# Kernel optimization log

Hardware: AMD Instinct MI355X
Metric: run time of the kernel (lower is better)

The kernel has to match this reference:

```python
import jax, jax.numpy as jnp
import numpy as np

INPUT_DIM = 1024
ATTN_DIM = 512
N1 = 4096
N2 = 4096


def setup_inputs() -> dict:
    key = jax.random.key(0)
    ks = jax.random.split(key, 10)
    s_in = 1.0 / np.sqrt(INPUT_DIM)   # torch Linear default init scale
    s_at = 1.0 / np.sqrt(ATTN_DIM)
    return {
        "input1": jax.random.normal(ks[0], (N1, INPUT_DIM), jnp.float32),
        "input2": jax.random.normal(ks[1], (N2, INPUT_DIM), jnp.float32),
        "Wq": jax.random.uniform(ks[2], (INPUT_DIM, ATTN_DIM), jnp.float32, -s_in, s_in),
        "bq": jax.random.uniform(ks[3], (ATTN_DIM,), jnp.float32, -s_in, s_in),
        "Wk": jax.random.uniform(ks[4], (INPUT_DIM, ATTN_DIM), jnp.float32, -s_in, s_in),
        "bk": jax.random.uniform(ks[5], (ATTN_DIM,), jnp.float32, -s_in, s_in),
        "Wv": jax.random.uniform(ks[6], (INPUT_DIM, ATTN_DIM), jnp.float32, -s_in, s_in),
        "bv": jax.random.uniform(ks[7], (ATTN_DIM,), jnp.float32, -s_in, s_in),
        "Wo": jax.random.uniform(ks[8], (ATTN_DIM, INPUT_DIM), jnp.float32, -s_at, s_at),
        "bo": jax.random.uniform(ks[9], (INPUT_DIM,), jnp.float32, -s_at, s_at),
    }


def reference(input1, input2, Wq, bq, Wk, bk, Wv, bv, Wo, bo):
    # shared projections for both inputs
    q1 = input1 @ Wq + bq            # [N1, A]
    q2 = input2 @ Wq + bq            # [N2, A]
    k1 = input1 @ Wk + bk
    k2 = input2 @ Wk + bk
    v1 = input1 @ Wv + bv
    v2 = input2 @ Wv + bv
    # cross attention 1: input1 queries attend to input2 keys/values
    attn1 = jax.nn.softmax(q1 @ k2.T, axis=-1)   # [N1, N2]
    attn2 = jax.nn.softmax(q2 @ k1.T, axis=-1)   # [N2, N1]
    out1 = (attn1 @ v2) @ Wo + bo                # [N1, input_dim]
    out2 = (attn2 @ v1) @ Wo + bo                # [N2, input_dim]
    return (out1, out2)
```

## Files before the change

### kernel.cpp

```cpp
#include <hip/hip_runtime.h>

typedef __bf16 bf16;
typedef _Float16 f16;
typedef __bf16 bf16x8 __attribute__((ext_vector_type(8)));
typedef _Float16 f16x8 __attribute__((ext_vector_type(8)));
typedef _Float16 f16x4 __attribute__((ext_vector_type(4)));
typedef float f32x4 __attribute__((ext_vector_type(4)));

#define NROWS 4096
#define DIN 1024
#define DA 512
#define NCHUNK 64

template <typename T> struct V8;
template <> struct V8<f16> { using type = f16x8; };
template <> struct V8<bf16> { using type = bf16x8; };

__device__ __forceinline__ f32x4 mfma16(f16x8 a, f16x8 b, f32x4 c) {
  return __builtin_amdgcn_mfma_f32_16x16x32_f16(a, b, c, 0, 0, 0);
}
__device__ __forceinline__ f32x4 mfma16(bf16x8 a, bf16x8 b, f32x4 c) {
  return __builtin_amdgcn_mfma_f32_16x16x32_bf16(a, b, c, 0, 0, 0);
}

__device__ __forceinline__ void gload_lds16(const void* g, void* l) {
  __builtin_amdgcn_global_load_lds((const __attribute__((address_space(1))) void*)g,
                                   (__attribute__((address_space(3))) void*)l, 16, 0, 0);
}

template <int N> __device__ __forceinline__ void vmcnt_wait() {
  if constexpr (N == 0) asm volatile("s_waitcnt vmcnt(0)" ::: "memory");
  else if constexpr (N == 1) asm volatile("s_waitcnt vmcnt(1)" ::: "memory");
  else if constexpr (N == 2) asm volatile("s_waitcnt vmcnt(2)" ::: "memory");
  else if constexpr (N == 3) asm volatile("s_waitcnt vmcnt(3)" ::: "memory");
  else if constexpr (N == 4) asm volatile("s_waitcnt vmcnt(4)" ::: "memory");
  else if constexpr (N == 5) asm volatile("s_waitcnt vmcnt(5)" ::: "memory");
  else if constexpr (N == 6) asm volatile("s_waitcnt vmcnt(6)" ::: "memory");
  else if constexpr (N == 8) asm volatile("s_waitcnt vmcnt(8)" ::: "memory");
  else static_assert(N == 0, "unsupported vmcnt");
}


__global__ void cast_kernel(const float* __restrict__ s1, const float* __restrict__ s2,
                            f16* __restrict__ d1, f16* __restrict__ d2, int n) {
  const float* s = blockIdx.z ? s2 : s1;
  f16* d = blockIdx.z ? d2 : d1;
  int i = (blockIdx.x * blockDim.x + threadIdx.x) * 4;
  if (i < n) {
    float4 v = *(const float4*)(s + i);
    f16x4 o;
    o[0] = (f16)v.x; o[1] = (f16)v.y; o[2] = (f16)v.z; o[3] = (f16)v.w;
    *(f16x4*)(d + i) = o;
  }
}

__global__ void transpose_f32(const float* __restrict__ w0, const float* __restrict__ w1,
                              const float* __restrict__ w2, f16* __restrict__ dst,
                              size_t dstride, int rows, int cols) {
  const float* s = blockIdx.z == 0 ? w0 : (blockIdx.z == 1 ? w1 : w2);
  f16* d = dst + (size_t)blockIdx.z * dstride;
  __shared__ float tile[32][33];
  int bc = blockIdx.x * 32, br = blockIdx.y * 32;
  int tx = threadIdx.x, ty = threadIdx.y;
  for (int i = ty; i < 32; i += 8)
    tile[i][tx] = s[(size_t)(br + i) * cols + bc + tx];
  __syncthreads();
  for (int i = ty; i < 32; i += 8)
    d[(size_t)(bc + i) * rows + br + tx] = (f16)tile[tx][i];
}

__global__ void transpose_b16(const bf16* __restrict__ src, size_t sstride,
                              bf16* __restrict__ dst, size_t dstride, int rows, int cols) {
  const bf16* s = src + (size_t)blockIdx.z * sstride;
  bf16* d = dst + (size_t)blockIdx.z * dstride;
  __shared__ float tile[32][33];
  int bc = blockIdx.x * 32, br = blockIdx.y * 32;
  int tx = threadIdx.x, ty = threadIdx.y;
  for (int i = ty; i < 32; i += 8)
    tile[i][tx] = (float)s[(size_t)(br + i) * cols + bc + tx];
  __syncthreads();
  for (int i = ty; i < 32; i += 8)
    d[(size_t)(bc + i) * rows + br + tx] = (bf16)tile[tx][i];
}

__global__ void rowsum_reduce(const float* __restrict__ prsP, float* __restrict__ prsT) {
  int i = blockIdx.x * 256 + threadIdx.x;
  int z = i >> 12, row = i & 4095;
  const float* p = prsP + (size_t)z * NCHUNK * NROWS + row;
  float s = 0.f;
#pragma unroll
  for (int j = 0; j < NCHUNK; ++j) s += p[(size_t)j * NROWS];
  prsT[i] = s;
}

__global__ void merge_kernel(const float* __restrict__ pO, const float* __restrict__ prsT,
                             f16* __restrict__ mid) {
  const size_t QS = (size_t)NROWS * DA;
  size_t e = ((size_t)blockIdx.x * blockDim.x + threadIdx.x) * 4;
  int z = (int)(e / QS);
  size_t rem = e - (size_t)z * QS;
  int row = (int)(rem / DA);
  float4 a = *(const float4*)(pO + (size_t)z * QS + rem);
  float4 b = *(const float4*)(pO + (size_t)(2 + z) * QS + rem);
  float inv = 1.0f / prsT[z * NROWS + row];
  f16x4 o;
  o[0] = (f16)((a.x + b.x) * inv);
  o[1] = (f16)((a.y + b.y) * inv);
  o[2] = (f16)((a.z + b.z) * inv);
  o[3] = (f16)((a.w + b.w) * inv);
  *(f16x4*)(mid + (size_t)z * QS + rem) = o;
}


template <typename TIN>
struct G8Args {
  const TIN* A[6];
  const TIN* B[6];
  const float* bias[6];
  void* C[6];
  float* rsO[6];
  int k0[6];
  int storebf[6];
  int lda, ldb, ldc;
};

template <typename TIN, int EPI, int BN, int NT, int BK = 64, int MINW = 1, int PH = 4>
__global__ __launch_bounds__(512, MINW) void g8(G8Args<TIN> args) {
  using vec8 = typename V8<TIN>::type;
  constexpr int NFR = BN / 64;
  constexpr int FPP = 8 / PH;
  constexpr int KK = BK / 32;
  constexpr int RB = BK * 2;
  constexpr int CPR = RB / 16;
  constexpr int SWM = CPR - 1;
  constexpr int SFT = (CPR == 4) ? 1 : 0;
  constexpr int ABUF = 256 * RB;
  constexpr int BBUF = BN * RB;
  constexpr int BUFSZ = ABUF + BBUF;
  constexpr int IPU = ABUF / 2 / 8192;
  __shared__ __align__(16) char smem[2 * BUFSZ];

  static_assert(PH == 4 || PH == 2, "PH in {2,4}");

  const int z = blockIdx.z;
  const TIN* __restrict__ A = args.A[z];
  const TIN* __restrict__ B = args.B[z];
  const int lda = args.lda, ldb = args.ldb;
  const int k0 = args.k0[z];

  int blkM, blkN;
  {
    const int gx = gridDim.x;
    const int nwg = gx * gridDim.y;
    const int lin = blockIdx.y * gx + blockIdx.x;
    const int q = nwg >> 3;
    const int nl = (lin & 7) * q + (lin >> 3);
    blkN = nl % gx;
    blkM = nl / gx;
  }

  const int tid = threadIdx.x;
  const int w = tid >> 6, lane = tid & 63;
  const int wm = w & 1, wn = w >> 1;
  const int lr = lane & 15, lh = lane >> 4;

  const TIN* Abase = A + (size_t)blkM * 256 * lda;
  const TIN* Bbase = B + (size_t)blkN * BN * ldb;

  f32x4 acc[8][NFR] = {};
  vec8 af[FPP][KK], bfr[NFR][KK];

#define SWZ(r_) (((r_) >> SFT) & SWM)
#define STAGE_A(buf, hf, kt)                                                    \
  {                                                                             \
    char* dst_ = smem + (buf)*BUFSZ + (hf)*(ABUF / 2);                          \
    const TIN* src_ = Abase + (size_t)((hf)*128) * lda + (kt);                  \
    _Pragma("unroll")                                                           \
    for (int i_ = 0; i_ < IPU; ++i_) {                                          \
      int c_ = i_ * 512 + tid;                                                  \
      int r_ = c_ / CPR, q_ = c_ % CPR;                                         \
      gload_lds16(src_ + (size_t)r_ * lda + ((q_ ^ SWZ(r_)) << 3),              \
                  dst_ + c_ * 16);                                              \
    }                                                                           \
  }
#define STAGE_B(buf, hf, kt)                                                    \
  {                                                                             \
    char* dst_ = smem + (buf)*BUFSZ + ABUF + (hf)*(ABUF / 2);                   \
    const TIN* src_ = Bbase + (size_t)((hf)*128) * ldb + (kt);                  \
    _Pragma("unroll")                                                           \
    for (int i_ = 0; i_ < IPU; ++i_) {                                          \
      int c_ = i_ * 512 + tid;                                                  \
      int r_ = c_ / CPR, q_ = c_ % CPR;                                         \
      gload_lds16(src_ + (size_t)r_ * ldb + ((q_ ^ SWZ(r_)) << 3),              \
                  dst_ + c_ * 16);                                              \
    }                                                                           \
  }
#define LDA_PHASE(buf, p)                                                       \
  {                                                                             \
    char* Ab_ = smem + (buf)*BUFSZ;                                             \
    _Pragma("unroll")                                                           \
    for (int fi_ = 0; fi_ < FPP; ++fi_) {                                       \
      int row_ = (((p)*FPP + fi_) * 2 + wm) * 16 + lr;                          \
      _Pragma("unroll")                                                         \
      for (int kk_ = 0; kk_ < KK; ++kk_) {                                      \
        int cc_ = (kk_ * 4 + lh) ^ SWZ(row_);                                   \
        af[fi_][kk_] = *(const vec8*)(Ab_ + row_ * RB + cc_ * 16);              \
      }                                                                         \
    }                                                                           \
  }
#define LDB_ALL(buf)                                                            \
  {                                                                             \
    char* Bb_ = smem + (buf)*BUFSZ + ABUF;                                      \
    _Pragma("unroll")                                                           \
    for (int n_ = 0; n_ < NFR; ++n_) {                                          \
      int row_ = wn * (BN / 4) + n_ * 16 + lr;                                  \
      _Pragma("unroll")                                                         \
      for (int kk_ = 0; kk_ < KK; ++kk_) {                                      \
        int cc_ = (kk_ * 4 + lh) ^ SWZ(row_);                                   \
        bfr[n_][kk_] = *(const vec8*)(Bb_ + row_ * RB + cc_ * 16);              \
      }                                                                         \
    }                                                                           \
  }
#define MFMA_PHASE(p)                                                           \
  {                                                                             \
    _Pragma("unroll")                                                           \
    for (int fi_ = 0; fi_ < FPP; ++fi_) {                                       \
      _Pragma("unroll")                                                         \
      for (int n_ = 0; n_ < NFR; ++n_) {                                        \
        _Pragma("unroll")                                                       \
        for (int kk_ = 0; kk_ < KK; ++kk_)                                      \
          acc[(p)*FPP + fi_][n_] = mfma16(af[fi_][kk_], bfr[n_][kk_],           \
                                          acc[(p)*FPP + fi_][n_]);              \
      }                                                                         \
    }                                                                           \
  }
#define BAR() __builtin_amdgcn_s_barrier()
#define LGK0()                                          \
  asm volatile("s_waitcnt lgkmcnt(0)" ::: "memory");    \
  __builtin_amdgcn_sched_barrier(0)

  if constexpr (NFR == 4) {
    STAGE_B(0, 0, k0); STAGE_B(0, 1, k0); STAGE_A(0, 0, k0); STAGE_A(0, 1, k0);
  } else {
    STAGE_B(0, 0, k0); STAGE_A(0, 0, k0); STAGE_A(0, 1, k0);
  }
  vmcnt_wait<IPU>();
  BAR();

  for (int t = 0; t < NT; ++t) {
    const int cur = t & 1, nxt = cur ^ 1;
    const int ktn = k0 + (t + 1) * BK;
    const bool st = (t < NT - 1);
    if constexpr (PH == 4) {
      if (st) { STAGE_B(nxt, 0, ktn); }
      LDB_ALL(cur);
      LDA_PHASE(cur, 0);
      BAR(); LGK0();
      __builtin_amdgcn_s_setprio(1); MFMA_PHASE(0); __builtin_amdgcn_s_setprio(0);
      BAR();
      if (st) { STAGE_B(nxt, 1, ktn); }
      LDA_PHASE(cur, 1);
      BAR(); LGK0();
      __builtin_amdgcn_s_setprio(1); MFMA_PHASE(1); __builtin_amdgcn_s_setprio(0);
      if (st) { vmcnt_wait<2 * IPU>(); }
      else    { vmcnt_wait<0>(); }
      BAR();
      if (st) { STAGE_A(nxt, 0, ktn); }
      LDA_PHASE(cur, 2);
      BAR(); LGK0();
      __builtin_amdgcn_s_setprio(1); MFMA_PHASE(2); __builtin_amdgcn_s_setprio(0);
      BAR();
      if (st) { STAGE_A(nxt, 1, ktn); }
      LDA_PHASE(cur, 3);
      BAR(); LGK0();
      __builtin_amdgcn_s_setprio(1); MFMA_PHASE(3); __builtin_amdgcn_s_setprio(0);
      if (st) { vmcnt_wait<IPU>(); }
      BAR();
    } else {
      if (st) {
        STAGE_B(nxt, 0, ktn);
        if constexpr (NFR == 4) { STAGE_B(nxt, 1, ktn); }
        STAGE_A(nxt, 0, ktn);
      }
      LDB_ALL(cur);
      LDA_PHASE(cur, 0);
      BAR(); LGK0();
      __builtin_amdgcn_s_setprio(1); MFMA_PHASE(0); __builtin_amdgcn_s_setprio(0);
      if (st) { vmcnt_wait<(NFR == 4 ? 3 : 2) * IPU>(); }
      else    { vmcnt_wait<0>(); }
      BAR();
      if (st) { STAGE_A(nxt, 1, ktn); }
      LDA_PHASE(cur, 1);
      BAR(); LGK0();
      __builtin_amdgcn_s_setprio(1); MFMA_PHASE(1); __builtin_amdgcn_s_setprio(0);
      if (st) { vmcnt_wait<IPU>(); }
      BAR();
    }
  }

  const int row0 = blkM * 256;
  const int col0 = blkN * BN + wn * (BN / 4);
  const int ldc = args.ldc;
  if constexpr (EPI == 1) {
#pragma unroll
    for (int a = 0; a < 8; ++a) {
      float rsv[4] = {0.f, 0.f, 0.f, 0.f};
#pragma unroll
      for (int n = 0; n < NFR; ++n) {
#pragma unroll
        for (int rr = 0; rr < 4; ++rr) {
          int row = row0 + (a * 2 + wm) * 16 + lh * 4 + rr;
          int col = col0 + n * 16 + lr;
          float e = __expf(acc[a][n][rr]);
          ((bf16*)args.C[z])[(size_t)row * ldc + col] = (bf16)e;
          rsv[rr] += e;
        }
      }
#pragma unroll
      for (int rr = 0; rr < 4; ++rr) {
        float s = rsv[rr];
        s += __shfl_xor(s, 1);
        s += __shfl_xor(s, 2);
        s += __shfl_xor(s, 4);
        s += __shfl_xor(s, 8);
        if (lr == 0) {
          int row = row0 + (a * 2 + wm) * 16 + lh * 4 + rr;
          args.rsO[z][((size_t)blkN * 4 + wn) * NROWS + row] = s;
        }
      }
    }
  } else {
#pragma unroll
    for (int a = 0; a < 8; ++a) {
#pragma unroll
      for (int n = 0; n < NFR; ++n) {
#pragma unroll
        for (int rr = 0; rr < 4; ++rr) {
          int row = row0 + (a * 2 + wm) * 16 + lh * 4 + rr;
          int col = col0 + n * 16 + lr;
          float v = acc[a][n][rr];
          if constexpr (EPI == 0) {
            float b = v + args.bias[z][col];
            if (args.storebf[z])
              ((bf16*)args.C[z])[(size_t)row * ldc + col] = (bf16)b;
            else
              ((f16*)args.C[z])[(size_t)row * ldc + col] = (f16)b;
          } else if constexpr (EPI == 2) {
            ((float*)args.C[z])[(size_t)row * ldc + col] = v;
          } else {
            ((float*)args.C[z])[(size_t)row * ldc + col] = v + args.bias[z][col];
          }
        }
      }
    }
  }
#undef SWZ
#undef STAGE_A
#undef STAGE_B
#undef LDA_PHASE
#undef LDB_ALL
#undef MFMA_PHASE
#undef BAR
#undef LGK0
}


extern "C" void kernel_launch(void* const* d_in, const int* in_sizes, int n_in,
                              void* d_out, int out_size, void* d_ws, size_t ws_size,
                              hipStream_t stream) {
  const float* in1 = (const float*)d_in[0];
  const float* in2 = (const float*)d_in[1];
  const float* Wq = (const float*)d_in[2];
  const float* bq = (const float*)d_in[3];
  const float* Wk = (const float*)d_in[4];
  const float* bk = (const float*)d_in[5];
  const float* Wv = (const float*)d_in[6];
  const float* bv = (const float*)d_in[7];
  const float* Wo = (const float*)d_in[8];
  const float* bo = (const float*)d_in[9];
  float* out = (float*)d_out;

  const size_t IN_E = (size_t)NROWS * DIN;
  const size_t WT_E = (size_t)DA * DIN;
  const size_t QS = (size_t)NROWS * DA;
  const size_t PS = (size_t)NROWS * NROWS;

  f16* qk = (f16*)d_ws;
  f16* in_hf = qk + 4 * QS;
  bf16* vv = (bf16*)(in_hf + 2 * IN_E);
  f16* wt = (f16*)(vv + 2 * QS);
  f16* woT = wt + 3 * WT_E;
  bf16* vt = (bf16*)(woT + WT_E);
  bf16* P = vt + 2 * QS;
  f16* mid = (f16*)(P + 2 * PS);
  float* pO = (float*)d_ws;
  float* prsP = (float*)vv;
  float* prsT = prsP + 2 * (size_t)NCHUNK * NROWS;

  cast_kernel<<<dim3((unsigned)(IN_E / 1024), 1, 2), dim3(256), 0, stream>>>(
      in1, in2, in_hf, in_hf + IN_E, (int)IN_E);

  transpose_f32<<<dim3(DA / 32, DIN / 32, 3), dim3(32, 8), 0, stream>>>(
      Wq, Wk, Wv, wt, WT_E, DIN, DA);
  transpose_f32<<<dim3(DIN / 32, DA / 32, 1), dim3(32, 8), 0, stream>>>(
      Wo, Wo, Wo, woT, 0, DA, DIN);

  {
    G8Args<f16> a{};
    const float* bs[3] = {bq, bk, bv};
    for (int zi = 0; zi < 6; ++zi) {
      int which = (zi < 4) ? (zi & 1) : 2;
      int src = (zi < 4) ? (zi >> 1) : (zi - 4);
      a.A[zi] = in_hf + (size_t)src * IN_E;
      a.B[zi] = wt + (size_t)which * WT_E;
      a.bias[zi] = bs[which];
      a.C[zi] = (zi < 4) ? (void*)(qk + (size_t)zi * QS) : (void*)(vv + (size_t)(zi - 4) * QS);
      a.storebf[zi] = (zi >= 4);
      a.k0[zi] = 0;
    }
    a.lda = DIN; a.ldb = DIN; a.ldc = DA;
    g8<f16, 0, 256, 16, 64, 1, 2><<<dim3(2, 16, 6), dim3(512), 0, stream>>>(a);
  }

  transpose_b16<<<dim3(DA / 32, NROWS / 32, 2), dim3(32, 8), 0, stream>>>(
      vv, QS, vt, QS, NROWS, DA);

  {
    G8Args<f16> a{};
    a.A[0] = qk + 0 * QS; a.B[0] = qk + 3 * QS; a.C[0] = P;
    a.A[1] = qk + 2 * QS; a.B[1] = qk + 1 * QS; a.C[1] = P + PS;
    a.rsO[0] = prsP;
    a.rsO[1] = prsP + (size_t)NCHUNK * NROWS;
    a.k0[0] = a.k0[1] = 0;
    a.lda = DA; a.ldb = DA; a.ldc = NROWS;
    g8<f16, 1, 256, 8, 64, 1, 2><<<dim3(16, 16, 2), dim3(512), 0, stream>>>(a);
  }

  rowsum_reduce<<<dim3(32), dim3(256), 0, stream>>>(prsP, prsT);

  {
    G8Args<bf16> a{};
    for (int i = 0; i < 4; ++i) {
      int pair = i & 1, s = i >> 1;
      a.A[i] = P + (size_t)pair * PS;
      a.B[i] = vt + (size_t)(pair ^ 1) * QS;
      a.C[i] = pO + (size_t)i * QS;
      a.k0[i] = s * 2048;
      a.storebf[i] = 0;
    }
    a.lda = NROWS; a.ldb = NROWS; a.ldc = DA;
    g8<bf16, 2, 128, 32, 64, 1, 2><<<dim3(4, 16, 4), dim3(512), 0, stream>>>(a);
  }

  merge_kernel<<<dim3((unsigned)(2 * QS / 1024)), dim3(256), 0, stream>>>(pO, prsT, mid);

  {
    G8Args<f16> a{};
    a.A[0] = mid;      a.C[0] = out;
    a.A[1] = mid + QS; a.C[1] = out + (size_t)NROWS * DIN;
    a.B[0] = a.B[1] = woT;
    a.bias[0] = a.bias[1] = bo;
    a.k0[0] = a.k0[1] = 0;
    a.lda = DA; a.ldb = DA; a.ldc = DIN;
    g8<f16, 3, 128, 8, 64, 1, 2><<<dim3(8, 16, 2), dim3(512), 0, stream>>>(a);
  }
}
```

Before: 203.7 us.

## Add dedicated QK^T exp kernel with 256x128 tiles and two blocks per CU

Replaces the generic g8 launch for the QK^T + exp + partial rowsum stage with a specialized kernel using 256x128 tiles, 48KB LDS, launch bounds allowing two blocks per CU, and a swizzled block order for L2 reuse. The column tile halves, so the number of partial rowsum chunks doubles (NCHUNK 64->128). The goal is more resident waves to hide latency and better scheduling of the exp-heavy epilogue. The cost is more blocks, reloading A tiles for every column block, and a larger rowsum reduction.

Result: slower. 233.0 us (+14.4%).

```diff
diff --git a/kernel.cpp b/kernel.cpp
--- a/kernel.cpp
+++ b/kernel.cpp
@@ -10,7 +10,7 @@
 #define NROWS 4096
 #define DIN 1024
 #define DA 512
-#define NCHUNK 64
+#define NCHUNK 128
 
 template <typename T> struct V8;
 template <> struct V8<f16> { using type = f16x8; };
@@ -109,6 +109,159 @@
   o[2] = (f16)((a.z + b.z) * inv);
   o[3] = (f16)((a.w + b.w) * inv);
   *(f16x4*)(mid + (size_t)z * QS + rem) = o;
+}
+
+
+__global__ __launch_bounds__(512, 2) void qk2(
+    const f16* __restrict__ q1, const f16* __restrict__ k2,
+    const f16* __restrict__ q2, const f16* __restrict__ k1,
+    bf16* __restrict__ Pout, float* __restrict__ prsP) {
+  __shared__ __align__(16) char smem[49152];
+  const int z = blockIdx.z;
+  const f16* __restrict__ A = z ? q2 : q1;
+  const f16* __restrict__ B = z ? k1 : k2;
+  bf16* __restrict__ C = Pout + (size_t)z * ((size_t)NROWS * NROWS);
+  float* __restrict__ rsO = prsP + (size_t)z * NCHUNK * NROWS;
+
+  int blkM, blkN;
+  {
+    const int lin = blockIdx.y * 32 + blockIdx.x;
+    const int nl = (lin & 7) * 64 + (lin >> 3);
+    blkN = nl & 31;
+    blkM = nl >> 5;
+  }
+
+  const int tid = threadIdx.x;
+  const int w = tid >> 6, lane = tid & 63;
+  const int wm = w & 1, wn = w >> 1;
+  const int lr = lane & 15, lh = lane >> 4;
+
+  const f16* Abase = A + (size_t)blkM * 256 * DA;
+  const f16* Bbase = B + (size_t)blkN * 128 * DA;
+
+  char* const bA0 = smem;
+  char* const bA1 = smem + 16384;
+  char* const bB = smem + 32768;
+
+  f32x4 acc[8][2] = {};
+  f16x8 af[4][2], bfr[2][2];
+
+#define STAGEU(dst_, src_)                                                      \
+  {                                                                             \
+    _Pragma("unroll")                                                           \
+    for (int i_ = 0; i_ < 2; ++i_) {                                            \
+      int c_ = i_ * 512 + tid;                                                  \
+      int r_ = c_ >> 3, q_ = c_ & 7;                                            \
+      gload_lds16((src_) + (size_t)r_ * DA + ((q_ ^ (r_ & 7)) << 3),            \
+                  (dst_) + c_ * 16);                                            \
+    }                                                                           \
+  }
+#define LDA_P(p)                                                                \
+  {                                                                             \
+    char* Ab_ = (p) ? bA1 : bA0;                                                \
+    _Pragma("unroll")                                                           \
+    for (int fi_ = 0; fi_ < 4; ++fi_) {                                         \
+      int grow_ = (((p)*4 + fi_) * 2 + wm) * 16 + lr;                           \
+      int row_ = grow_ & 127;                                                   \
+      _Pragma("unroll")                                                         \
+      for (int kk_ = 0; kk_ < 2; ++kk_) {                                       \
+        int cc_ = (kk_ * 4 + lh) ^ (row_ & 7);                                  \
+        af[fi_][kk_] = *(const f16x8*)(Ab_ + row_ * 128 + cc_ * 16);            \
+      }                                                                         \
+    }                                                                           \
+  }
+#define LDB_ALL()                                                               \
+  {                                                                             \
+    _Pragma("unroll")                                                           \
+    for (int n_ = 0; n_ < 2; ++n_) {                                            \
+      int row_ = wn * 32 + n_ * 16 + lr;                                        \
+      _Pragma("unroll")                                                         \
+      for (int kk_ = 0; kk_ < 2; ++kk_) {                                       \
+        int cc_ = (kk_ * 4 + lh) ^ (row_ & 7);                                  \
+        bfr[n_][kk_] = *(const f16x8*)(bB + row_ * 128 + cc_ * 16);             \
+      }                                                                         \
+    }                                                                           \
+  }
+#define MFMA_P(p)                                                               \
+  {                                                                             \
+    _Pragma("unroll")                                                           \
+    for (int fi_ = 0; fi_ < 4; ++fi_) {                                         \
+      _Pragma("unroll")                                                         \
+      for (int n_ = 0; n_ < 2; ++n_) {                                          \
+        _Pragma("unroll")                                                       \
+        for (int kk_ = 0; kk_ < 2; ++kk_)                                       \
+          acc[(p)*4 + fi_][n_] = mfma16(af[fi_][kk_], bfr[n_][kk_],             \
+                                        acc[(p)*4 + fi_][n_]);                  \
+      }                                                                         \
+    }                                                                           \
+  }
+#define BAR() __builtin_amdgcn_s_barrier()
+#define LGK0()                                          \
+  asm volatile("s_waitcnt lgkmcnt(0)" ::: "memory");    \
+  __builtin_amdgcn_sched_barrier(0)
+
+  STAGEU(bB, Bbase);
+  STAGEU(bA0, Abase);
+
+  for (int t = 0; t < 8; ++t) {
+    const int kt = t * 64;
+    const bool st = (t < 7);
+    STAGEU(bA1, Abase + (size_t)128 * DA + kt);
+    vmcnt_wait<2>();
+    BAR();
+    LDB_ALL();
+    LDA_P(0);
+    LGK0();
+    __builtin_amdgcn_s_setprio(1); MFMA_P(0); __builtin_amdgcn_s_setprio(0);
+    BAR();
+    if (st) {
+      STAGEU(bB, Bbase + kt + 64);
+      STAGEU(bA0, Abase + kt + 64);
+    }
+    if (st) { vmcnt_wait<4>(); }
+    else    { vmcnt_wait<0>(); }
+    BAR();
+    LDA_P(1);
+    LGK0();
+    __builtin_amdgcn_s_setprio(1); MFMA_P(1); __builtin_amdgcn_s_setprio(0);
+    BAR();
+  }
+
+  const int row0 = blkM * 256;
+  const int col0 = blkN * 128 + wn * 32;
+#pragma unroll
+  for (int a = 0; a < 8; ++a) {
+    float rsv[4] = {0.f, 0.f, 0.f, 0.f};
+#pragma unroll
+    for (int n = 0; n < 2; ++n) {
+#pragma unroll
+      for (int rr = 0; rr < 4; ++rr) {
+        int row = row0 + (a * 2 + wm) * 16 + lh * 4 + rr;
+        int col = col0 + n * 16 + lr;
+        float e = __expf(acc[a][n][rr]);
+        C[(size_t)row * NROWS + col] = (bf16)e;
+        rsv[rr] += e;
+      }
+    }
+#pragma unroll
+    for (int rr = 0; rr < 4; ++rr) {
+      float s = rsv[rr];
+      s += __shfl_xor(s, 1);
+      s += __shfl_xor(s, 2);
+      s += __shfl_xor(s, 4);
+      s += __shfl_xor(s, 8);
+      if (lr == 0) {
+        int row = row0 + (a * 2 + wm) * 16 + lh * 4 + rr;
+        rsO[((size_t)blkN * 4 + wn) * NROWS + row] = s;
+      }
+    }
+  }
+#undef STAGEU
+#undef LDA_P
+#undef LDB_ALL
+#undef MFMA_P
+#undef BAR
+#undef LGK0
 }
 
 
@@ -301,55 +454,25 @@
   const int row0 = blkM * 256;
   const int col0 = blkN * BN + wn * (BN / 4);
   const int ldc = args.ldc;
-  if constexpr (EPI == 1) {
-#pragma unroll
-    for (int a = 0; a < 8; ++a) {
-      float rsv[4] = {0.f, 0.f, 0.f, 0.f};
-#pragma unroll
-      for (int n = 0; n < NFR; ++n) {
-#pragma unroll
-        for (int rr = 0; rr < 4; ++rr) {
-          int row = row0 + (a * 2 + wm) * 16 + lh * 4 + rr;
-          int col = col0 + n * 16 + lr;
-          float e = __expf(acc[a][n][rr]);
-          ((bf16*)args.C[z])[(size_t)row * ldc + col] = (bf16)e;
-          rsv[rr] += e;
-        }
-      }
+#pragma unroll
+  for (int a = 0; a < 8; ++a) {
+#pragma unroll
+    for (int n = 0; n < NFR; ++n) {
 #pragma unroll
       for (int rr = 0; rr < 4; ++rr) {
-        float s = rsv[rr];
-        s += __shfl_xor(s, 1);
-        s += __shfl_xor(s, 2);
-        s += __shfl_xor(s, 4);
-        s += __shfl_xor(s, 8);
-        if (lr == 0) {
-          int row = row0 + (a * 2 + wm) * 16 + lh * 4 + rr;
-          args.rsO[z][((size_t)blkN * 4 + wn) * NROWS + row] = s;
-        }
-      }
-    }
-  } else {
-#pragma unroll
-    for (int a = 0; a < 8; ++a) {
-#pragma unroll
-      for (int n = 0; n < NFR; ++n) {
-#pragma unroll
-        for (int rr = 0; rr < 4; ++rr) {
-          int row = row0 + (a * 2 + wm) * 16 + lh * 4 + rr;
-          int col = col0 + n * 16 + lr;
-          float v = acc[a][n][rr];
-          if constexpr (EPI == 0) {
-            float b = v + args.bias[z][col];
-            if (args.storebf[z])
-              ((bf16*)args.C[z])[(size_t)row * ldc + col] = (bf16)b;
-            else
-              ((f16*)args.C[z])[(size_t)row * ldc + col] = (f16)b;
-          } else if constexpr (EPI == 2) {
-            ((float*)args.C[z])[(size_t)row * ldc + col] = v;
-          } else {
-            ((float*)args.C[z])[(size_t)row * ldc + col] = v + args.bias[z][col];
-          }
+        int row = row0 + (a * 2 + wm) * 16 + lh * 4 + rr;
+        int col = col0 + n * 16 + lr;
+        float v = acc[a][n][rr];
+        if constexpr (EPI == 0) {
+          float b = v + args.bias[z][col];
+          if (args.storebf[z])
+            ((bf16*)args.C[z])[(size_t)row * ldc + col] = (bf16)b;
+          else
+            ((f16*)args.C[z])[(size_t)row * ldc + col] = (f16)b;
+        } else if constexpr (EPI == 2) {
+          ((float*)args.C[z])[(size_t)row * ldc + col] = v;
+        } else {
+          ((float*)args.C[z])[(size_t)row * ldc + col] = v + args.bias[z][col];
         }
       }
     }
@@ -425,16 +548,8 @@
   transpose_b16<<<dim3(DA / 32, NROWS / 32, 2), dim3(32, 8), 0, stream>>>(
       vv, QS, vt, QS, NROWS, DA);
 
-  {
-    G8Args<f16> a{};
-    a.A[0] = qk + 0 * QS; a.B[0] = qk + 3 * QS; a.C[0] = P;
-    a.A[1] = qk + 2 * QS; a.B[1] = qk + 1 * QS; a.C[1] = P + PS;
-    a.rsO[0] = prsP;
-    a.rsO[1] = prsP + (size_t)NCHUNK * NROWS;
-    a.k0[0] = a.k0[1] = 0;
-    a.lda = DA; a.ldb = DA; a.ldc = NROWS;
-    g8<f16, 1, 256, 8, 64, 1, 2><<<dim3(16, 16, 2), dim3(512), 0, stream>>>(a);
-  }
+  qk2<<<dim3(32, 16, 2), dim3(512), 0, stream>>>(
+      qk + 0 * QS, qk + 3 * QS, qk + 2 * QS, qk + 1 * QS, P, prsP);
 
   rowsum_reduce<<<dim3(32), dim3(256), 0, stream>>>(prsP, prsT);
 
```

## Fuse V transpose into projection epilogue and softmax normalization into PV epilogue

Applied to the files above, without the earlier changes.

The projection GEMM now writes V already transposed, staging the tile through swizzled shared memory and storing it with vectorized writes. This removes the separate transpose_b16 kernel and its round trip through memory. The PV GEMM epilogue divides by the row sums and stores f16 partials instead of f32, which halves the partial traffic and lets the merge kernel do only an 8-wide add. In exchange, precision drops because each split-K partial is rounded to f16 before the sum.

After: 192.2 us. 1.06x faster.

```diff
diff --git a/kernel.cpp b/kernel.cpp
--- a/kernel.cpp
+++ b/kernel.cpp
@@ -6,6 +6,7 @@
 typedef _Float16 f16x8 __attribute__((ext_vector_type(8)));
 typedef _Float16 f16x4 __attribute__((ext_vector_type(4)));
 typedef float f32x4 __attribute__((ext_vector_type(4)));
+typedef unsigned int u32x4 __attribute__((ext_vector_type(4)));
 
 #define NROWS 4096
 #define DIN 1024
@@ -69,20 +70,6 @@
     d[(size_t)(bc + i) * rows + br + tx] = (f16)tile[tx][i];
 }
 
-__global__ void transpose_b16(const bf16* __restrict__ src, size_t sstride,
-                              bf16* __restrict__ dst, size_t dstride, int rows, int cols) {
-  const bf16* s = src + (size_t)blockIdx.z * sstride;
-  bf16* d = dst + (size_t)blockIdx.z * dstride;
-  __shared__ float tile[32][33];
-  int bc = blockIdx.x * 32, br = blockIdx.y * 32;
-  int tx = threadIdx.x, ty = threadIdx.y;
-  for (int i = ty; i < 32; i += 8)
-    tile[i][tx] = (float)s[(size_t)(br + i) * cols + bc + tx];
-  __syncthreads();
-  for (int i = ty; i < 32; i += 8)
-    d[(size_t)(bc + i) * rows + br + tx] = (bf16)tile[tx][i];
-}
-
 __global__ void rowsum_reduce(const float* __restrict__ prsP, float* __restrict__ prsT) {
   int i = blockIdx.x * 256 + threadIdx.x;
   int z = i >> 12, row = i & 4095;
@@ -93,22 +80,17 @@
   prsT[i] = s;
 }
 
-__global__ void merge_kernel(const float* __restrict__ pO, const float* __restrict__ prsT,
-                             f16* __restrict__ mid) {
+__global__ void merge_kernel(const f16* __restrict__ pO, f16* __restrict__ mid) {
   const size_t QS = (size_t)NROWS * DA;
-  size_t e = ((size_t)blockIdx.x * blockDim.x + threadIdx.x) * 4;
+  size_t e = ((size_t)blockIdx.x * blockDim.x + threadIdx.x) * 8;
   int z = (int)(e / QS);
   size_t rem = e - (size_t)z * QS;
-  int row = (int)(rem / DA);
-  float4 a = *(const float4*)(pO + (size_t)z * QS + rem);
-  float4 b = *(const float4*)(pO + (size_t)(2 + z) * QS + rem);
-  float inv = 1.0f / prsT[z * NROWS + row];
-  f16x4 o;
-  o[0] = (f16)((a.x + b.x) * inv);
-  o[1] = (f16)((a.y + b.y) * inv);
-  o[2] = (f16)((a.z + b.z) * inv);
-  o[3] = (f16)((a.w + b.w) * inv);
-  *(f16x4*)(mid + (size_t)z * QS + rem) = o;
+  f16x8 a = *(const f16x8*)(pO + (size_t)z * QS + rem);
+  f16x8 b = *(const f16x8*)(pO + (size_t)(2 + z) * QS + rem);
+  f16x8 o;
+#pragma unroll
+  for (int j = 0; j < 8; ++j) o[j] = (f16)((float)a[j] + (float)b[j]);
+  *(f16x8*)(mid + (size_t)z * QS + rem) = o;
 }
 
 
@@ -329,6 +311,61 @@
         }
       }
     }
+  } else if constexpr (EPI == 2) {
+#pragma unroll
+    for (int a = 0; a < 8; ++a) {
+#pragma unroll
+      for (int rr = 0; rr < 4; ++rr) {
+        int row = row0 + (a * 2 + wm) * 16 + lh * 4 + rr;
+        float rinv = 1.0f / args.rsO[z][row];
+#pragma unroll
+        for (int n = 0; n < NFR; ++n) {
+          int col = col0 + n * 16 + lr;
+          ((f16*)args.C[z])[(size_t)row * ldc + col] = (f16)(acc[a][n][rr] * rinv);
+        }
+      }
+    }
+  } else if constexpr (EPI == 0 && BN == 256) {
+    if (args.storebf[z]) {
+#pragma unroll
+      for (int a = 0; a < 8; ++a) {
+#pragma unroll
+        for (int n = 0; n < NFR; ++n) {
+#pragma unroll
+          for (int rr = 0; rr < 4; ++rr) {
+            int row_l = (a * 2 + wm) * 16 + lh * 4 + rr;
+            int col_l = wn * 64 + n * 16 + lr;
+            float b = acc[a][n][rr] + args.bias[z][blkN * 256 + col_l];
+            int byte = col_l * 512 + (((row_l >> 3) ^ (col_l & 31)) << 4) + (row_l & 7) * 2;
+            *(bf16*)(smem + byte) = (bf16)b;
+          }
+        }
+      }
+      __syncthreads();
+      bf16* vt = (bf16*)args.C[z];
+#pragma unroll
+      for (int i = 0; i < 16; ++i) {
+        int cidx = i * 512 + tid;
+        int c = cidx >> 5, ch = cidx & 31;
+        u32x4 v = *(const u32x4*)(smem + c * 512 + ((ch ^ (c & 31)) << 4));
+        size_t dst = (size_t)(blkN * 256 + c) * NROWS + blkM * 256 + ch * 8;
+        *(u32x4*)(vt + dst) = v;
+      }
+    } else {
+#pragma unroll
+      for (int a = 0; a < 8; ++a) {
+#pragma unroll
+        for (int n = 0; n < NFR; ++n) {
+#pragma unroll
+          for (int rr = 0; rr < 4; ++rr) {
+            int row = row0 + (a * 2 + wm) * 16 + lh * 4 + rr;
+            int col = col0 + n * 16 + lr;
+            ((f16*)args.C[z])[(size_t)row * ldc + col] =
+                (f16)(acc[a][n][rr] + args.bias[z][col]);
+          }
+        }
+      }
+    }
   } else {
 #pragma unroll
     for (int a = 0; a < 8; ++a) {
@@ -340,13 +377,7 @@
           int col = col0 + n * 16 + lr;
           float v = acc[a][n][rr];
           if constexpr (EPI == 0) {
-            float b = v + args.bias[z][col];
-            if (args.storebf[z])
-              ((bf16*)args.C[z])[(size_t)row * ldc + col] = (bf16)b;
-            else
-              ((f16*)args.C[z])[(size_t)row * ldc + col] = (f16)b;
-          } else if constexpr (EPI == 2) {
-            ((float*)args.C[z])[(size_t)row * ldc + col] = v;
+            ((f16*)args.C[z])[(size_t)row * ldc + col] = (f16)(v + args.bias[z][col]);
           } else {
             ((float*)args.C[z])[(size_t)row * ldc + col] = v + args.bias[z][col];
           }
@@ -393,7 +424,7 @@
   bf16* vt = (bf16*)(woT + WT_E);
   bf16* P = vt + 2 * QS;
   f16* mid = (f16*)(P + 2 * PS);
-  float* pO = (float*)d_ws;
+  f16* pO = (f16*)d_ws;
   float* prsP = (float*)vv;
   float* prsT = prsP + 2 * (size_t)NCHUNK * NROWS;
 
@@ -414,16 +445,13 @@
       a.A[zi] = in_hf + (size_t)src * IN_E;
       a.B[zi] = wt + (size_t)which * WT_E;
       a.bias[zi] = bs[which];
-      a.C[zi] = (zi < 4) ? (void*)(qk + (size_t)zi * QS) : (void*)(vv + (size_t)(zi - 4) * QS);
+      a.C[zi] = (zi < 4) ? (void*)(qk + (size_t)zi * QS) : (void*)(vt + (size_t)(zi - 4) * QS);
       a.storebf[zi] = (zi >= 4);
       a.k0[zi] = 0;
     }
     a.lda = DIN; a.ldb = DIN; a.ldc = DA;
     g8<f16, 0, 256, 16, 64, 1, 2><<<dim3(2, 16, 6), dim3(512), 0, stream>>>(a);
   }
-
-  transpose_b16<<<dim3(DA / 32, NROWS / 32, 2), dim3(32, 8), 0, stream>>>(
-      vv, QS, vt, QS, NROWS, DA);
 
   {
     G8Args<f16> a{};
@@ -445,6 +473,7 @@
       a.A[i] = P + (size_t)pair * PS;
       a.B[i] = vt + (size_t)(pair ^ 1) * QS;
       a.C[i] = pO + (size_t)i * QS;
+      a.rsO[i] = prsT + (size_t)pair * NROWS;
       a.k0[i] = s * 2048;
       a.storebf[i] = 0;
     }
@@ -452,7 +481,7 @@
     g8<bf16, 2, 128, 32, 64, 1, 2><<<dim3(4, 16, 4), dim3(512), 0, stream>>>(a);
   }
 
-  merge_kernel<<<dim3((unsigned)(2 * QS / 1024)), dim3(256), 0, stream>>>(pO, prsT, mid);
+  merge_kernel<<<dim3((unsigned)(2 * QS / 2048)), dim3(256), 0, stream>>>(pO, mid);
 
   {
     G8Args<f16> a{};
```
